# Kernel tuning notes

Measured on AMD Instinct MI355X. Metric: run time of the kernel, lower is better.

The kernel has to match this reference:

```python
import jax, jax.numpy as jnp
import numpy as np

STACK_DEPTH = 16
SHARPEN = 5.0
LN_EPS = 1e-5
EPS = 1e-8


def _apply_tools(x, tw):
    # tools: relu, gelu(exact), tanh, sigmoid, identity; tw: [B, 5]
    return (jax.nn.relu(x) * tw[:, 0:1]
            + jax.nn.gelu(x, approximate=False) * tw[:, 1:2]
            + jnp.tanh(x) * tw[:, 2:3]
            + jax.nn.sigmoid(x) * tw[:, 3:4]
            + x * tw[:, 4:5])


def _forward(hidden_states, W_proj, b_proj, W_op, b_op, W_tool, b_tool, ln_gamma, ln_beta):
    B, S, H = hidden_states.shape
    D = STACK_DEPTH

    # Per-timestep linear ops are time-independent -> batch them up front.
    proj = jnp.einsum('bsh,ph->bsp', hidden_states, W_proj) + b_proj  # [B,S,2H]
    h_all, v_all = proj[..., :H], proj[..., H:]
    op_probs = jax.nn.softmax(jnp.einsum('bsh,oh->bso', hidden_states, W_op) + b_op, axis=-1)  # [B,S,3]
    tool_w = jax.nn.softmax(jnp.einsum('bsh,th->bst', h_all, W_tool) + b_tool, axis=-1)  # [B,S,T]

    # Differentiable stack recurrence (push/pop/nop with pointer sharpening).
    stack0 = jnp.zeros((B, D, H), hidden_states.dtype)
    pointer0 = jnp.zeros((B, D), hidden_states.dtype).at[:, 0].set(1.0)

    def step(carry, xs):
        stack, pointer = carry
        value, ops = xs  # value: [B,H], ops: [B,3]
        push, pop, nop = ops[:, 0:1], ops[:, 1:2], ops[:, 2:3]
        p_push = jnp.roll(pointer, 1, axis=1)   # pointer moves up on push
        p_pop = jnp.roll(pointer, -1, axis=1)   # pointer moves down on pop
        new_p = push * p_push + pop * p_pop + nop * pointer
        new_p = new_p ** SHARPEN
        new_p = new_p / (jnp.sum(new_p, axis=1, keepdims=True) + EPS)
        w = (push * p_push)[..., None]          # [B,D,1] write weight at pushed slot
        new_stack = stack * (1.0 - w) + value[:, None, :] * w
        top = jnp.sum(new_stack * new_p[..., None], axis=1)  # [B,H]
        return (new_stack, new_p), top

    (stack_f, pointer_f), tops = jax.lax.scan(
        step, (stack0, pointer0),
        (jnp.swapaxes(v_all, 0, 1), jnp.swapaxes(op_probs, 0, 1)))
    tops = jnp.swapaxes(tops, 0, 1)  # [B,S,H]

    processed = jax.vmap(_apply_tools, in_axes=(1, 1), out_axes=1)(tops, tool_w)  # [B,S,H]
    combined = h_all + processed + hidden_states

    mu = jnp.mean(combined, axis=-1, keepdims=True)
    var = jnp.mean((combined - mu) ** 2, axis=-1, keepdims=True)
    final = (combined - mu) * jax.lax.rsqrt(var + LN_EPS) * ln_gamma + ln_beta
    return final, stack_f, pointer_f, tool_w


def setup_inputs() -> dict:
    key = jax.random.key(0)
    ks = jax.random.split(key, 4)
    B, S, H, T = 16, 2048, 1024, 5
    sd = 1.0 / np.sqrt(H)
    return {
        'hidden_states': jax.random.normal(ks[0], (B, S, H), jnp.float32),
        'W_proj': jax.random.normal(ks[1], (2 * H, H), jnp.float32) * sd,
        'b_proj': jnp.zeros((2 * H,), jnp.float32),
        'W_op': jax.random.normal(ks[2], (3, H), jnp.float32) * sd,
        'b_op': jnp.zeros((3,), jnp.float32),
        'W_tool': jax.random.normal(ks[3], (T, H), jnp.float32) * sd,
        'b_tool': jnp.zeros((T,), jnp.float32),
        'ln_gamma': jnp.ones((H,), jnp.float32),
        'ln_beta': jnp.zeros((H,), jnp.float32),
    }


def reference(hidden_states, W_proj, b_proj, W_op, b_op, W_tool, b_tool, ln_gamma, ln_beta):
    return _forward(hidden_states, W_proj, b_proj, W_op, b_op, W_tool, b_tool, ln_gamma, ln_beta)
```

## Files before the change

kernel.cpp:

```cpp
#include <hip/hip_runtime.h>
#include <hip/hip_bf16.h>
#include <cstdint>
#include <cstdio>


typedef float f32x4 __attribute__((ext_vector_type(4)));
typedef __bf16 bf8v __attribute__((ext_vector_type(8)));

#define WS_ABF   0ULL
#define WS_WBF   67108864ULL
#define WS_PROJ  71303168ULL
#define WS_OP4   205520896ULL
#define WS_WP    206045184ULL
#define WS_NEED  210239488ULL

#define OUT_FINAL 0
#define OUT_STACK 33554432ULL
#define OUT_PTR   33816576ULL
#define OUT_TOOLW 33816832ULL
#define SLE_OFF    0ULL
#define SSTART_OFF 9437184ULL
#define COEF_OFF   18874368ULL
#define ATOT_OFF   30000000ULL

__device__ __forceinline__ float bf2f(unsigned short u) {
    union { unsigned int i; float f; } v; v.i = ((unsigned int)u) << 16; return v.f;
}
__device__ __forceinline__ unsigned short f2bf(float f) {
    __hip_bfloat16 h = __float2bfloat16(f);
    return __builtin_bit_cast(unsigned short, h);
}
template<int C>
__device__ __forceinline__ float fdpp(float x) {
    return __int_as_float(__builtin_amdgcn_mov_dpp(__float_as_int(x), C, 0xF, 0xF, true));
}
__device__ __forceinline__ void gload_lds16(const void* g, void* l) {
    __builtin_amdgcn_global_load_lds(
        (__attribute__((address_space(1))) void*)(uintptr_t)g,
        (__attribute__((address_space(3))) void*)l,
        16, 0, 0);
}

__global__ __launch_bounds__(256) void k0(const float* __restrict__ hid,
                                          const float* __restrict__ Wp,
                                          const float* __restrict__ Wop,
                                          const float* __restrict__ bop,
                                          unsigned short* __restrict__ Abf,
                                          unsigned short* __restrict__ Wbf,
                                          float4* __restrict__ op4)
{
    const int bid = blockIdx.x, tid = threadIdx.x;
    if (bid < 8192) {
        const int wid = tid >> 6, lane = tid & 63;
        const int row = bid * 4 + wid;
        const float* hrow = hid + (size_t)row * 1024 + lane * 16;
        float xs[16];
        #pragma unroll
        for (int j = 0; j < 4; ++j) {
            float4 t = *(const float4*)(hrow + j * 4);
            xs[j*4+0] = t.x; xs[j*4+1] = t.y; xs[j*4+2] = t.z; xs[j*4+3] = t.w;
        }
        unsigned short us[16];
        #pragma unroll
        for (int j = 0; j < 16; ++j) us[j] = f2bf(xs[j]);
        uint4 ulo, uhi;
        ulo.x = (unsigned)us[0]  | ((unsigned)us[1]  << 16);
        ulo.y = (unsigned)us[2]  | ((unsigned)us[3]  << 16);
        ulo.z = (unsigned)us[4]  | ((unsigned)us[5]  << 16);
        ulo.w = (unsigned)us[6]  | ((unsigned)us[7]  << 16);
        uhi.x = (unsigned)us[8]  | ((unsigned)us[9]  << 16);
        uhi.y = (unsigned)us[10] | ((unsigned)us[11] << 16);
        uhi.z = (unsigned)us[12] | ((unsigned)us[13] << 16);
        uhi.w = (unsigned)us[14] | ((unsigned)us[15] << 16);
        unsigned short* arow = Abf + (size_t)row * 1024 + lane * 16;
        *(uint4*)(arow)     = ulo;
        *(uint4*)(arow + 8) = uhi;
        float pt[3] = {0.f, 0.f, 0.f};
        #pragma unroll
        for (int o = 0; o < 3; ++o) {
            const float* wrow = Wop + o * 1024 + lane * 16;
            #pragma unroll
            for (int j = 0; j < 4; ++j) {
                float4 t = *(const float4*)(wrow + j * 4);
                pt[o] += xs[j*4+0]*t.x + xs[j*4+1]*t.y + xs[j*4+2]*t.z + xs[j*4+3]*t.w;
            }
        }
        #pragma unroll
        for (int o = 0; o < 3; ++o)
            #pragma unroll
            for (int m = 32; m >= 1; m >>= 1) pt[o] += __shfl_xor(pt[o], m);
        if (lane == 0) {
            float l0 = pt[0] + bop[0], l1 = pt[1] + bop[1], l2 = pt[2] + bop[2];
            float mx = fmaxf(l0, fmaxf(l1, l2));
            float e0 = expf(l0 - mx), e1 = expf(l1 - mx), e2 = expf(l2 - mx);
            float inv = 1.0f / (e0 + e1 + e2);
            float4 r; r.x = e0 * inv; r.y = e1 * inv; r.z = e2 * inv; r.w = 0.f;
            op4[row] = r;
        }
    } else {
        const int b2 = bid - 8192;
        const size_t base = (size_t)b2 * 2048 + tid * 8;
        float4 a = *(const float4*)(Wp + base);
        float4 b = *(const float4*)(Wp + base + 4);
        unsigned short vs[8] = { f2bf(a.x), f2bf(a.y), f2bf(a.z), f2bf(a.w),
                                 f2bf(b.x), f2bf(b.y), f2bf(b.z), f2bf(b.w) };
        uint4 u;
        u.x = (unsigned)vs[0] | ((unsigned)vs[1] << 16);
        u.y = (unsigned)vs[2] | ((unsigned)vs[3] << 16);
        u.z = (unsigned)vs[4] | ((unsigned)vs[5] << 16);
        u.w = (unsigned)vs[6] | ((unsigned)vs[7] << 16);
        *(uint4*)(Wbf + base) = u;
    }
}

__global__ __launch_bounds__(512, 2) void k1(const unsigned short* __restrict__ Abf,
                                             const unsigned short* __restrict__ Wbf,
                                             const float* __restrict__ bproj,
                                             unsigned short* __restrict__ proj,
                                             const float4* __restrict__ op4,
                                             float* __restrict__ wpbuf,
                                             float* __restrict__ out)
{
    __shared__ uint4 sm[8192];
    const int bid = blockIdx.x, tid = threadIdx.x;

    if (bid < 16) {
        const int b = bid;
        #pragma unroll
        for (int i = 0; i < 4; ++i)
            sm[tid + i * 512] = ((const uint4*)op4)[(size_t)b * 2048 + tid + i * 512];
        __syncthreads();
        if (tid >= 64) return;
        __builtin_amdgcn_s_setprio(1);
        const int lane = tid, d = lane & 15;
        const float probe = (float)d;
        const bool ror1_is_push = (fdpp<0x121>(probe) == (float)((d + 15) & 15));
        float p = (d == 0) ? 1.0f : 0.0f;
        float Apre = 1.0f;
        const float4* smf = (const float4*)sm;
        float4 o0 = smf[0], o1 = smf[1];
        float* wpb = wpbuf + (size_t)b * 2048 * 32;
        float* atot = out + ATOT_OFF + (size_t)b * 32 * 16;
        #pragma unroll 2
        for (int s = 0; s < 2048; ++s) {
            float4 o2 = smf[(s + 2 < 2048) ? (s + 2) : 2047];
            const float push = o0.x, pop = o0.y, nop = o0.z;
            const float ra = fdpp<0x121>(p);
            const float rb = fdpp<0x12F>(p);
            const float ppush = ror1_is_push ? ra : rb;
            const float ppop  = ror1_is_push ? rb : ra;
            const float w = push * ppush;
            float lin = push * ppush + pop * ppop + nop * p;
            float x2 = lin * lin;
            float x5 = x2 * x2 * lin;
            float sum = x5;
            sum += fdpp<0x128>(sum);
            sum += fdpp<0x124>(sum);
            sum += fdpp<0x122>(sum);
            sum += fdpp<0x121>(sum);
            float pn = x5 * __builtin_amdgcn_rcpf(sum + 1e-8f);
            const float om = 1.0f - w;
            Apre = ((s & 63) == 0) ? om : Apre * om;
            if (lane < 16) {
                float2 wp; wp.x = w; wp.y = pn;
                *(float2*)(wpb + ((size_t)s * 16 + d) * 2) = wp;
                if ((s & 63) == 63) atot[(s >> 6) * 16 + d] = Apre;
            }
            p = pn;
            o0 = o1; o1 = o2;
        }
        if (lane < 16) out[OUT_PTR + (size_t)b * 16 + d] = p;
        return;
    }

    const int li = bid - 16;
    const int xcd = li & 7, j = li >> 3;
    const int gm = xcd * 16 + (j >> 3);
    const int gn = j & 7;
    const int wid = tid >> 6, lane = tid & 63;
    const int wm = wid >> 2, wn = wid & 3;
    const size_t row0 = (size_t)gm * 256;
    const size_t col0 = (size_t)gn * 256;
    char* smc = (char*)sm;
    const char* Ab = (const char*)Abf;
    const char* Bb = (const char*)Wbf;
    const int laneR = lane & 15;
    const int laneK = (lane >> 4) * 16;

    f32x4 acc[8][4];
    const f32x4 z = {0.f, 0.f, 0.f, 0.f};
    #pragma unroll
    for (int i = 0; i < 8; ++i)
        #pragma unroll
        for (int jj = 0; jj < 4; ++jj) acc[i][jj] = z;

    auto STAGE = [&](int kt, int slot) {
        #pragma unroll
        for (int hf = 0; hf < 4; ++hf) {
            #pragma unroll
            for (int i = 0; i < 2; ++i) {
                const int idx  = i * 512 + tid;
                const int off  = idx * 16;
                const int soff = off ^ (((off >> 7) & 7) << 4);
                const int irow = soff >> 7;
                const int colb = soff & 127;
                const char* src = (hf < 2)
                    ? (Ab + (row0 + (size_t)(hf * 128 + irow)) * 2048 + (size_t)kt * 128 + colb)
                    : (Bb + (col0 + (size_t)((hf - 2) * 128 + irow)) * 2048 + (size_t)kt * 128 + colb);
                gload_lds16(src, smc + slot * 65536 + hf * 16384 + (i * 512 + wid * 64) * 16);
            }
        }
    };

    STAGE(0, 0);
    int cur = 0;
    #pragma unroll 1
    for (int kt = 0; kt < 16; ++kt) {
        if (kt < 15) {
            STAGE(kt + 1, cur ^ 1);
            asm volatile("s_waitcnt vmcnt(8)" ::: "memory");
        } else {
            asm volatile("s_waitcnt vmcnt(0)" ::: "memory");
        }
        __builtin_amdgcn_sched_barrier(0);
        __builtin_amdgcn_s_barrier();
        const char* Abase = smc + cur * 65536 + wm * 16384;
        const char* Bbase = smc + cur * 65536 + 32768 + (wn >> 1) * 16384;
        const int bro = (wn & 1) * 64;

        bf8v af[4][2], bfr[4][2];
        #pragma unroll
        for (int m2 = 0; m2 < 4; ++m2)
            #pragma unroll
            for (int kk = 0; kk < 2; ++kk) {
                int byt = (m2 * 16 + laneR) * 128 + kk * 64 + laneK;
                byt ^= ((byt >> 7) & 7) << 4;
                af[m2][kk] = *(const bf8v*)(Abase + byt);
            }
        #pragma unroll
        for (int n2 = 0; n2 < 2; ++n2)
            #pragma unroll
            for (int kk = 0; kk < 2; ++kk) {
                int byt = (bro + n2 * 16 + laneR) * 128 + kk * 64 + laneK;
                byt ^= ((byt >> 7) & 7) << 4;
                bfr[n2][kk] = *(const bf8v*)(Bbase + byt);
            }
        __builtin_amdgcn_s_setprio(1);
        #pragma unroll
        for (int m2 = 0; m2 < 4; ++m2)
            #pragma unroll
            for (int n2 = 0; n2 < 2; ++n2)
                #pragma unroll
                for (int kk = 0; kk < 2; ++kk)
                    acc[m2][n2] = __builtin_amdgcn_mfma_f32_16x16x32_bf16(af[m2][kk], bfr[n2][kk], acc[m2][n2], 0, 0, 0);
        __builtin_amdgcn_s_setprio(0);
        __builtin_amdgcn_s_barrier();
        #pragma unroll
        for (int n2 = 2; n2 < 4; ++n2)
            #pragma unroll
            for (int kk = 0; kk < 2; ++kk) {
                int byt = (bro + n2 * 16 + laneR) * 128 + kk * 64 + laneK;
                byt ^= ((byt >> 7) & 7) << 4;
                bfr[n2][kk] = *(const bf8v*)(Bbase + byt);
            }
        __builtin_amdgcn_s_setprio(1);
        #pragma unroll
        for (int m2 = 0; m2 < 4; ++m2)
            #pragma unroll
            for (int n2 = 2; n2 < 4; ++n2)
                #pragma unroll
                for (int kk = 0; kk < 2; ++kk)
                    acc[m2][n2] = __builtin_amdgcn_mfma_f32_16x16x32_bf16(af[m2][kk], bfr[n2][kk], acc[m2][n2], 0, 0, 0);
        __builtin_amdgcn_s_setprio(0);
        __builtin_amdgcn_s_barrier();
        #pragma unroll
        for (int m2 = 0; m2 < 4; ++m2)
            #pragma unroll
            for (int kk = 0; kk < 2; ++kk) {
                int byt = ((64 + m2 * 16 + laneR)) * 128 + kk * 64 + laneK;
                byt ^= ((byt >> 7) & 7) << 4;
                af[m2][kk] = *(const bf8v*)(Abase + byt);
            }
        __builtin_amdgcn_s_setprio(1);
        #pragma unroll
        for (int m2 = 0; m2 < 4; ++m2)
            #pragma unroll
            for (int n2 = 2; n2 < 4; ++n2)
                #pragma unroll
                for (int kk = 0; kk < 2; ++kk)
                    acc[4 + m2][n2] = __builtin_amdgcn_mfma_f32_16x16x32_bf16(af[m2][kk], bfr[n2][kk], acc[4 + m2][n2], 0, 0, 0);
        __builtin_amdgcn_s_setprio(0);
        __builtin_amdgcn_s_barrier();
        __builtin_amdgcn_s_setprio(1);
        #pragma unroll
        for (int m2 = 0; m2 < 4; ++m2)
            #pragma unroll
            for (int n2 = 0; n2 < 2; ++n2)
                #pragma unroll
                for (int kk = 0; kk < 2; ++kk)
                    acc[4 + m2][n2] = __builtin_amdgcn_mfma_f32_16x16x32_bf16(af[m2][kk], bfr[n2][kk], acc[4 + m2][n2], 0, 0, 0);
        __builtin_amdgcn_s_setprio(0);
        __builtin_amdgcn_s_barrier();
        cur ^= 1;
    }
    #pragma unroll
    for (int mr = 0; mr < 8; ++mr) {
        const int rloc = wm * 128 + mr * 16 + ((lane >> 4) * 4);
        #pragma unroll
        for (int nr = 0; nr < 4; ++nr) {
            const size_t col = col0 + wn * 64 + nr * 16 + laneR;
            const float bias = bproj[col];
            #pragma unroll
            for (int jj = 0; jj < 4; ++jj)
                proj[(row0 + rloc + jj) * 2048 + col] = f2bf(acc[mr][nr][jj] + bias);
        }
    }
}

__global__ __launch_bounds__(256) void k2(unsigned short* __restrict__ proj,
                                          const float* __restrict__ wpbuf,
                                          float* __restrict__ sle)
{
    __shared__ unsigned short vlds[2][4096];
    const int bid = blockIdx.x, tid = threadIdx.x;
    const int hg = bid & 3, c = (bid >> 2) & 31, b = bid >> 7;
    const int wid = tid >> 6;
    const char* vbase = (const char*)proj +
        ((size_t)(b * 2048 + c * 64) * 2048 + 1024 + hg * 256) * 2;
    const float* wpb = wpbuf + ((size_t)b * 2048 + c * 64) * 32;
    unsigned short* topb = proj + ((size_t)b * 2048 + c * 64) * 2048 + 1024 + hg * 256 + tid;

    float st[16];
    #pragma unroll
    for (int d = 0; d < 16; ++d) st[d] = 0.f;

    auto STAGE = [&](int sc, int buf) {
        #pragma unroll
        for (int i = 0; i < 2; ++i) {
            const int g = i * 256 + tid;
            gload_lds16(vbase + (size_t)(sc * 16 + (g >> 5)) * 4096 + (g & 31) * 16,
                        (char*)vlds + buf * 8192 + (i * 256 + wid * 64) * 16);
        }
    };
    STAGE(0, 0);
    __syncthreads();
    for (int sc = 0; sc < 4; ++sc) {
        const int cur = sc & 1;
        if (sc < 3) STAGE(sc + 1, cur ^ 1);
        const unsigned short* vl = vlds[cur];
        #pragma unroll 4
        for (int ls = 0; ls < 16; ++ls) {
            const float v = bf2f(vl[ls * 256 + tid]);
            const float4* wp4 = (const float4*)(wpb + (size_t)(sc * 16 + ls) * 32);
            float t0 = 0.f, t1 = 0.f;
            #pragma unroll
            for (int k = 0; k < 8; ++k) {
                float4 q = wp4[k];
                st[2*k]   = fmaf(q.x, v - st[2*k],   st[2*k]);
                st[2*k+1] = fmaf(q.z, v - st[2*k+1], st[2*k+1]);
                t0 = fmaf(q.y, st[2*k],   t0);
                t1 = fmaf(q.w, st[2*k+1], t1);
            }
            topb[(size_t)(sc * 16 + ls) * 2048] = f2bf(t0 + t1);
        }
        __syncthreads();
    }
    float* so = sle + ((size_t)b * 32 + c) * 16 * 1024 + hg * 256 + tid;
    #pragma unroll
    for (int d = 0; d < 16; ++d) so[(size_t)d * 1024] = st[d];
}

__global__ __launch_bounds__(64) void k2c(const float* __restrict__ wpbuf,
                                          float* __restrict__ coefb)
{
    const int bid = blockIdx.x, tid = threadIdx.x;
    if (tid >= 16) return;
    const int b = bid >> 5, c = bid & 31;
    const float* wp = wpbuf + (size_t)b * 65536 + (size_t)c * 64 * 32 + tid * 2;
    float* co = coefb + (size_t)bid * 1024 + tid;
    float A = 1.f;
    #pragma unroll 8
    for (int j = 0; j < 64; ++j) {
        float2 q = *(const float2*)(wp + j * 32);
        A *= (1.f - q.x);
        co[j * 16] = q.y * A;
    }
}

__global__ __launch_bounds__(256) void k2b(const float* __restrict__ sle,
                                           const float* __restrict__ atot,
                                           float* __restrict__ sstart)
{
    const int bid = blockIdx.x, tid = threadIdx.x;
    const int hg = bid & 3, d = (bid >> 2) & 15, b = bid >> 6;
    const int h = hg * 256 + tid;
    const float* sb = sle    + ((size_t)b * 512 + d) * 1024 + h;
    float*       so = sstart + ((size_t)b * 512 + d) * 1024 + h;
    const float* ab = atot + (size_t)b * 512 + d;
    float st = 0.f;
    #pragma unroll 4
    for (int c = 0; c < 31; ++c) {
        so[(size_t)c * 16384] = st;
        st = fmaf(ab[c * 16], st, sb[(size_t)c * 16384]);
    }
    so[31ull * 16384] = st;
}

__global__ __launch_bounds__(256) void k3p(unsigned short* __restrict__ proj,
                                           const float* __restrict__ sstart,
                                           const float* __restrict__ coefb,
                                           const float* __restrict__ sle,
                                           const float* __restrict__ atot,
                                           float* __restrict__ out)
{
    __shared__ float ssL[16384];
    __shared__ float cofL[1024];
    const int bid = blockIdx.x, tid = threadIdx.x;
    const int b = bid >> 5, c = bid & 31;
    {
        const float4* ssg = (const float4*)(sstart + (size_t)bid * 16384);
        #pragma unroll
        for (int i = 0; i < 16; ++i)
            ((float4*)ssL)[i * 256 + tid] = ssg[i * 256 + tid];
        ((float4*)cofL)[tid] = ((const float4*)(coefb + (size_t)bid * 1024))[tid];
    }
    __syncthreads();
    const int h0 = tid * 4;
    float ss[16][4];
    #pragma unroll
    for (int d = 0; d < 16; ++d) {
        float4 t = *(const float4*)(ssL + d * 1024 + h0);
        ss[d][0] = t.x; ss[d][1] = t.y; ss[d][2] = t.z; ss[d][3] = t.w;
    }
    unsigned short* trow = proj + ((size_t)(b * 2048 + c * 64)) * 2048 + 1024 + h0;
    #pragma unroll 2
    for (int s = 0; s < 64; ++s) {
        uint2 tu = *(const uint2*)(trow + (size_t)s * 2048);
        float a0 = bf2f(tu.x & 0xffff), a1 = bf2f(tu.x >> 16);
        float a2 = bf2f(tu.y & 0xffff), a3 = bf2f(tu.y >> 16);
        #pragma unroll
        for (int d = 0; d < 16; ++d) {
            const float cf = cofL[s * 16 + d];
            a0 = fmaf(cf, ss[d][0], a0);
            a1 = fmaf(cf, ss[d][1], a1);
            a2 = fmaf(cf, ss[d][2], a2);
            a3 = fmaf(cf, ss[d][3], a3);
        }
        uint2 o;
        o.x = (unsigned)f2bf(a0) | ((unsigned)f2bf(a1) << 16);
        o.y = (unsigned)f2bf(a2) | ((unsigned)f2bf(a3) << 16);
        *(uint2*)(trow + (size_t)s * 2048) = o;
    }
    if (c == 31) {
        #pragma unroll
        for (int d = 0; d < 16; ++d) {
            float4 sl = *(const float4*)(sle + (((size_t)b * 32 + 31) * 16 + d) * 1024 + h0);
            const float A = atot[(size_t)b * 512 + 31 * 16 + d];
            float4 r;
            r.x = fmaf(A, ss[d][0], sl.x); r.y = fmaf(A, ss[d][1], sl.y);
            r.z = fmaf(A, ss[d][2], sl.z); r.w = fmaf(A, ss[d][3], sl.w);
            *(float4*)(out + OUT_STACK + ((size_t)b * 16 + d) * 1024 + h0) = r;
        }
    }
}

__global__ __launch_bounds__(256) void k5(const unsigned short* __restrict__ proj,
                                          const unsigned short* __restrict__ hidbf,
                                          const float* __restrict__ Wtool,
                                          const float* __restrict__ btool,
                                          const float* __restrict__ gamma,
                                          const float* __restrict__ beta,
                                          float* __restrict__ out)
{
    __shared__ float red[4][8];
    const int row = blockIdx.x, tid = threadIdx.x;
    const int wid = tid >> 6, lane = tid & 63;
    const int k0i = tid * 4;
    uint2 hu = *(const uint2*)(proj + (size_t)row * 2048 + k0i);
    float hh[4];
    hh[0] = bf2f(hu.x & 0xffff); hh[1] = bf2f(hu.x >> 16);
    hh[2] = bf2f(hu.y & 0xffff); hh[3] = bf2f(hu.y >> 16);
    uint2 tu = *(const uint2*)(proj + (size_t)row * 2048 + 1024 + k0i);
    float xs[4];
    xs[0] = bf2f(tu.x & 0xffff); xs[1] = bf2f(tu.x >> 16);
    xs[2] = bf2f(tu.y & 0xffff); xs[3] = bf2f(tu.y >> 16);
    uint2 du = *(const uint2*)(hidbf + (size_t)row * 1024 + k0i);
    float hds[4];
    hds[0] = bf2f(du.x & 0xffff); hds[1] = bf2f(du.x >> 16);
    hds[2] = bf2f(du.y & 0xffff); hds[3] = bf2f(du.y >> 16);
    float pt[5];
    #pragma unroll
    for (int t = 0; t < 5; ++t) {
        float4 wv = *(const float4*)(Wtool + t * 1024 + k0i);
        pt[t] = hh[0]*wv.x + hh[1]*wv.y + hh[2]*wv.z + hh[3]*wv.w;
    }
    #pragma unroll
    for (int t = 0; t < 5; ++t)
        #pragma unroll
        for (int m = 32; m >= 1; m >>= 1) pt[t] += __shfl_xor(pt[t], m);
    if (lane == 0) {
        #pragma unroll
        for (int t = 0; t < 5; ++t) red[wid][t] = pt[t];
    }
    __syncthreads();
    float tw[5];
    {
        float lg[5];
        #pragma unroll
        for (int t = 0; t < 5; ++t)
            lg[t] = red[0][t] + red[1][t] + red[2][t] + red[3][t] + btool[t];
        float mx = fmaxf(fmaxf(fmaxf(lg[0], lg[1]), fmaxf(lg[2], lg[3])), lg[4]);
        float se = 0.f;
        #pragma unroll
        for (int t = 0; t < 5; ++t) { tw[t] = expf(lg[t] - mx); se += tw[t]; }
        float inv = 1.0f / se;
        #pragma unroll
        for (int t = 0; t < 5; ++t) tw[t] *= inv;
    }
    if (tid < 5) out[OUT_TOOLW + (size_t)row * 5 + tid] = tw[tid];
    float cj[4];
    #pragma unroll
    for (int j = 0; j < 4; ++j) {
        const float x = xs[j];
        const float rl = fmaxf(x, 0.f);
        const float gl = 0.5f * x * (1.f + erff(x * 0.70710678118654752f));
        const float th = tanhf(x);
        const float sg = 1.f / (1.f + expf(-x));
        const float pr = rl*tw[0] + gl*tw[1] + th*tw[2] + sg*tw[3] + x*tw[4];
        cj[j] = hh[j] + pr + hds[j];
    }
    float s1 = cj[0] + cj[1] + cj[2] + cj[3];
    float s2 = cj[0]*cj[0] + cj[1]*cj[1] + cj[2]*cj[2] + cj[3]*cj[3];
    #pragma unroll
    for (int m = 32; m >= 1; m >>= 1) { s1 += __shfl_xor(s1, m); s2 += __shfl_xor(s2, m); }
    __syncthreads();
    if (lane == 0) { red[wid][0] = s1; red[wid][1] = s2; }
    __syncthreads();
    const float S1 = red[0][0] + red[1][0] + red[2][0] + red[3][0];
    const float S2 = red[0][1] + red[1][1] + red[2][1] + red[3][1];
    const float mu = S1 * (1.f / 1024.f);
    const float var = S2 * (1.f / 1024.f) - mu * mu;
    const float rstd = rsqrtf(var + 1e-5f);
    float4 g4 = *(const float4*)(gamma + k0i);
    float4 b4 = *(const float4*)(beta + k0i);
    float4 res;
    res.x = (cj[0] - mu) * rstd * g4.x + b4.x;
    res.y = (cj[1] - mu) * rstd * g4.y + b4.y;
    res.z = (cj[2] - mu) * rstd * g4.z + b4.z;
    res.w = (cj[3] - mu) * rstd * g4.w + b4.w;
    *(float4*)(out + (size_t)row * 1024 + k0i) = res;
}

extern "C" void kernel_launch(void* const* d_in, const int* in_sizes, int n_in,
                              void* d_out, int out_size, void* d_ws, size_t ws_size,
                              hipStream_t stream)
{
    if (ws_size < WS_NEED) {
        fprintf(stderr, "kernel_launch: ws_size %zu < required %llu\n",
                ws_size, (unsigned long long)WS_NEED);
        return;
    }
    const float* hid = (const float*)d_in[0];
    const float* Wp  = (const float*)d_in[1];
    const float* bp  = (const float*)d_in[2];
    const float* Wop = (const float*)d_in[3];
    const float* bop = (const float*)d_in[4];
    const float* Wtl = (const float*)d_in[5];
    const float* btl = (const float*)d_in[6];
    const float* gam = (const float*)d_in[7];
    const float* bet = (const float*)d_in[8];
    float* out = (float*)d_out;
    char* ws = (char*)d_ws;
    unsigned short* Abf  = (unsigned short*)(ws + WS_ABF);
    unsigned short* Wbf  = (unsigned short*)(ws + WS_WBF);
    unsigned short* proj = (unsigned short*)(ws + WS_PROJ);
    float4* op4 = (float4*)(ws + WS_OP4);
    float* wpbuf = (float*)(ws + WS_WP);
    float* sle    = out + SLE_OFF;
    float* sstart = out + SSTART_OFF;
    float* coefb  = out + COEF_OFF;
    float* atot   = out + ATOT_OFF;

    k0 <<<9216, 256, 0, stream>>>(hid, Wp, Wop, bop, Abf, Wbf, op4);
    k1 <<<1040, 512, 0, stream>>>(Abf, Wbf, bp, proj, op4, wpbuf, out);
    k2 <<<2048, 256, 0, stream>>>(proj, wpbuf, sle);
    k2c<<<512,  64,  0, stream>>>(wpbuf, coefb);
    k2b<<<1024, 256, 0, stream>>>(sle, atot, sstart);
    k3p<<<512,  256, 0, stream>>>(proj, sstart, coefb, sle, atot, out);
    k5 <<<32768, 256, 0, stream>>>(proj, Abf, Wtl, btl, gam, bet, out);
}
```

Before: 473.6 us.

## Pack four batches per recurrence wavefront and fuse coefficient computation into it

The pointer recurrence now runs four batch elements per 64-lane wavefront (16 lanes each) in 4 blocks instead of 16 blocks that each left 48 lanes idle. The DPP direction is resolved at compile time through template specialisation, removing per-step selects. The separate k2c kernel that computed pn*cumulative-product coefficients is folded into the recurrence loop, which saves one launch and one reread of wpbuf. The serial recurrence now shares its wavefront slot with more work and does an extra store per step, which could lengthen the critical path if it overlaps poorly with the GEMM blocks.

```diff
diff --git a/kernel.cpp b/kernel.cpp
--- a/kernel.cpp
+++ b/kernel.cpp
@@ -2,6 +2,7 @@
 #include <hip/hip_bf16.h>
 #include <cstdint>
 #include <cstdio>
+#include <type_traits>
 
 
 typedef float f32x4 __attribute__((ext_vector_type(4)));
@@ -124,56 +125,64 @@
     __shared__ uint4 sm[8192];
     const int bid = blockIdx.x, tid = threadIdx.x;
 
-    if (bid < 16) {
-        const int b = bid;
-        #pragma unroll
-        for (int i = 0; i < 4; ++i)
-            sm[tid + i * 512] = ((const uint4*)op4)[(size_t)b * 2048 + tid + i * 512];
+    if (bid < 4) {
+        const int bbase = bid * 4;
+        #pragma unroll
+        for (int i = 0; i < 16; ++i)
+            sm[tid + i * 512] = ((const uint4*)op4)[(size_t)bbase * 2048 + tid + i * 512];
         __syncthreads();
         if (tid >= 64) return;
         __builtin_amdgcn_s_setprio(1);
-        const int lane = tid, d = lane & 15;
+        const int lane = tid, d = lane & 15, b4 = lane >> 4;
+        const int b = bbase + b4;
+        const float4* smf = (const float4*)sm + (size_t)b4 * 2048;
+        float* wpb  = wpbuf + (size_t)b * 65536;
+        float* cob  = out + COEF_OFF + (size_t)b * 32768;
+        float* atot = out + ATOT_OFF + (size_t)b * 512;
         const float probe = (float)d;
         const bool ror1_is_push = (fdpp<0x121>(probe) == (float)((d + 15) & 15));
         float p = (d == 0) ? 1.0f : 0.0f;
         float Apre = 1.0f;
-        const float4* smf = (const float4*)sm;
-        float4 o0 = smf[0], o1 = smf[1];
-        float* wpb = wpbuf + (size_t)b * 2048 * 32;
-        float* atot = out + ATOT_OFF + (size_t)b * 32 * 16;
-        #pragma unroll 2
-        for (int s = 0; s < 2048; ++s) {
-            float4 o2 = smf[(s + 2 < 2048) ? (s + 2) : 2047];
-            const float push = o0.x, pop = o0.y, nop = o0.z;
-            const float ra = fdpp<0x121>(p);
-            const float rb = fdpp<0x12F>(p);
-            const float ppush = ror1_is_push ? ra : rb;
-            const float ppop  = ror1_is_push ? rb : ra;
-            const float w = push * ppush;
-            float lin = push * ppush + pop * ppop + nop * p;
-            float x2 = lin * lin;
-            float x5 = x2 * x2 * lin;
-            float sum = x5;
-            sum += fdpp<0x128>(sum);
-            sum += fdpp<0x124>(sum);
-            sum += fdpp<0x122>(sum);
-            sum += fdpp<0x121>(sum);
-            float pn = x5 * __builtin_amdgcn_rcpf(sum + 1e-8f);
-            const float om = 1.0f - w;
-            Apre = ((s & 63) == 0) ? om : Apre * om;
-            if (lane < 16) {
+
+        auto run = [&](auto pushc, auto popc) {
+            constexpr int PU = decltype(pushc)::value;
+            constexpr int PO = decltype(popc)::value;
+            float4 o0 = smf[0], o1 = smf[1];
+            #pragma unroll 4
+            for (int s = 0; s < 2048; ++s) {
+                float4 o2 = smf[(s + 2 < 2048) ? (s + 2) : 2047];
+                const float push = o0.x, pop = o0.y, nop = o0.z;
+                const float ppush = fdpp<PU>(p);
+                const float ppop  = fdpp<PO>(p);
+                const float w = push * ppush;
+                float lin = push * ppush + pop * ppop + nop * p;
+                float x2 = lin * lin;
+                float x5 = x2 * x2 * lin;
+                float sum = x5;
+                sum += fdpp<0x128>(sum);
+                sum += fdpp<0x124>(sum);
+                sum += fdpp<0x122>(sum);
+                sum += fdpp<0x121>(sum);
+                float pn = x5 * __builtin_amdgcn_rcpf(sum + 1e-8f);
+                const float om = 1.0f - w;
+                Apre = ((s & 63) == 0) ? om : Apre * om;
                 float2 wp; wp.x = w; wp.y = pn;
                 *(float2*)(wpb + ((size_t)s * 16 + d) * 2) = wp;
+                cob[(size_t)s * 16 + d] = pn * Apre;
                 if ((s & 63) == 63) atot[(s >> 6) * 16 + d] = Apre;
-            }
-            p = pn;
-            o0 = o1; o1 = o2;
-        }
-        if (lane < 16) out[OUT_PTR + (size_t)b * 16 + d] = p;
+                p = pn;
+                o0 = o1; o1 = o2;
+            }
+        };
+        if (ror1_is_push)
+            run(std::integral_constant<int,0x121>{}, std::integral_constant<int,0x12F>{});
+        else
+            run(std::integral_constant<int,0x12F>{}, std::integral_constant<int,0x121>{});
+        out[OUT_PTR + (size_t)b * 16 + d] = p;
         return;
     }
 
-    const int li = bid - 16;
+    const int li = bid - 4;
     const int xcd = li & 7, j = li >> 3;
     const int gm = xcd * 16 + (j >> 3);
     const int gn = j & 7;
@@ -368,23 +377,6 @@
     float* so = sle + ((size_t)b * 32 + c) * 16 * 1024 + hg * 256 + tid;
     #pragma unroll
     for (int d = 0; d < 16; ++d) so[(size_t)d * 1024] = st[d];
-}
-
-__global__ __launch_bounds__(64) void k2c(const float* __restrict__ wpbuf,
-                                          float* __restrict__ coefb)
-{
-    const int bid = blockIdx.x, tid = threadIdx.x;
-    if (tid >= 16) return;
-    const int b = bid >> 5, c = bid & 31;
-    const float* wp = wpbuf + (size_t)b * 65536 + (size_t)c * 64 * 32 + tid * 2;
-    float* co = coefb + (size_t)bid * 1024 + tid;
-    float A = 1.f;
-    #pragma unroll 8
-    for (int j = 0; j < 64; ++j) {
-        float2 q = *(const float2*)(wp + j * 32);
-        A *= (1.f - q.x);
-        co[j * 16] = q.y * A;
-    }
 }
 
 __global__ __launch_bounds__(256) void k2b(const float* __restrict__ sle,
@@ -582,9 +574,8 @@
     float* atot   = out + ATOT_OFF;
 
     k0 <<<9216, 256, 0, stream>>>(hid, Wp, Wop, bop, Abf, Wbf, op4);
-    k1 <<<1040, 512, 0, stream>>>(Abf, Wbf, bp, proj, op4, wpbuf, out);
+    k1 <<<1028, 512, 0, stream>>>(Abf, Wbf, bp, proj, op4, wpbuf, out);
     k2 <<<2048, 256, 0, stream>>>(proj, wpbuf, sle);
-    k2c<<<512,  64,  0, stream>>>(wpbuf, coefb);
     k2b<<<1024, 256, 0, stream>>>(sle, atot, sstart);
     k3p<<<512,  256, 0, stream>>>(proj, sstart, coefb, sle, atot, out);
     k5 <<<32768, 256, 0, stream>>>(proj, Abf, Wtl, btl, gam, bet, out);
```

Measured after the change: 450.5 us, median of 3. -4.9%, faster.
